# Kernel tuning notes

Hardware: AMD Instinct MI355X
Metric: run time of the kernel (lower is better)

The kernel has to match this reference:

```python
import jax, jax.numpy as jnp
import numpy as np

B, N, DIM = 64, 197, 768
NUM_HEAD, HEAD_DIM = 12, 64
SCALE = HEAD_DIM ** -0.5
WS = (14, 14)
NUM_REL = (2 * WS[0] - 1) * (2 * WS[1] - 1) + 3  # 732


def _relative_position_index():
    coords = np.stack(np.meshgrid(np.arange(WS[0]), np.arange(WS[1]), indexing='ij'))  # (2, Wh, Ww)
    cf = coords.reshape(2, -1)                              # (2, Wh*Ww)
    rel = (cf[:, :, None] - cf[:, None, :]).transpose(1, 2, 0).astype(np.int64)
    rel[:, :, 0] += WS[0] - 1
    rel[:, :, 1] += WS[1] - 1
    rel[:, :, 0] *= 2 * WS[1] - 1
    idx = np.zeros((WS[0] * WS[1] + 1,) * 2, dtype=np.int32)
    idx[1:, 1:] = rel.sum(-1)
    idx[0, :] = NUM_REL - 3
    idx[:, 0] = NUM_REL - 2
    idx[0, 0] = NUM_REL - 1
    return idx


def setup_inputs() -> dict:
    key = jax.random.key(0)
    k1, k2, k3, k4 = jax.random.split(key, 4)
    x = jax.random.normal(k1, (B, N, DIM), dtype=jnp.float32)
    qkv_w = jax.random.normal(k2, (3 * DIM, DIM), dtype=jnp.float32) * (DIM ** -0.5)
    q_bias = jnp.zeros((DIM,), dtype=jnp.float32)
    v_bias = jnp.zeros((DIM,), dtype=jnp.float32)
    rpb_table = jax.random.normal(k3, (NUM_REL, NUM_HEAD), dtype=jnp.float32) * 0.02
    proj_w = jax.random.normal(k4, (DIM, DIM), dtype=jnp.float32) * (DIM ** -0.5)
    proj_b = jnp.zeros((DIM,), dtype=jnp.float32)
    rel_index = jnp.asarray(_relative_position_index())
    return {"x": x, "qkv_w": qkv_w, "q_bias": q_bias, "v_bias": v_bias,
            "rpb_table": rpb_table, "proj_w": proj_w, "proj_b": proj_b,
            "rel_index": rel_index}


def reference(x, qkv_w, q_bias, v_bias, rpb_table, proj_w, proj_b, rel_index):
    b, n, c = x.shape
    # qkv projection with [q_bias, 0, v_bias] bias layout
    qkv_bias = jnp.concatenate([q_bias, jnp.zeros_like(v_bias), v_bias])
    qkv = x @ qkv_w.T + qkv_bias                               # (B, N, 3*C)
    qkv = qkv.reshape(b, n, 3, NUM_HEAD, HEAD_DIM).transpose(2, 0, 3, 1, 4)
    q, k, v = qkv[0] * SCALE, qkv[1], qkv[2]                   # (B, H, N, hd)
    attn = jnp.einsum('bhqd,bhkd->bhqk', q, k)                 # (B, H, N, N)
    # relative position bias gather: table[(N,N)] -> (N, N, H) -> (H, N, N)
    bias = rpb_table[rel_index].transpose(2, 0, 1)
    attn = jax.nn.softmax(attn + bias[None], axis=-1)
    out = jnp.einsum('bhqk,bhkd->bhqd', attn, v)               # (B, H, N, hd)
    out = out.transpose(0, 2, 1, 3).reshape(b, n, -1)
    return out @ proj_w.T + proj_b
```

## Files before the change

kernel.cpp:

```cpp
#include <hip/hip_runtime.h>


#define B_    64
#define N_    197
#define DIM_  768
#define H_    12
#define HD_   64
#define M_TOT (B_ * N_)

#define ST_A0   0
#define ST_A1   13312
#define ST_A2   26624
#define ST_B0   39936
#define ST_B1   52224
#define ST_B2   64512
#define OFF_Q   0
#define OFF_K   13312
#define OFF_VT  26624
#define LDS_TOT 76800

typedef __attribute__((ext_vector_type(8))) short bf8;
typedef __attribute__((ext_vector_type(4))) float f4;
typedef __attribute__((ext_vector_type(4))) unsigned short us4;

__device__ __forceinline__ unsigned short f2bf(float f) {
    unsigned u = __float_as_uint(f);
    u = (u + 0x7fffu + ((u >> 16) & 1u)) >> 16;
    return (unsigned short)u;
}

__device__ __forceinline__ void gl2lds16(const unsigned short* g, unsigned short* l) {
    __builtin_amdgcn_global_load_lds(
        (const __attribute__((address_space(1))) void*)g,
        (__attribute__((address_space(3))) void*)l, 16, 0, 0);
}

__device__ __forceinline__ int qkaddr(int row, int col) {
    return row * 64 + ((((col >> 3) ^ row) & 7) << 3) + (col & 7);
}
__device__ __forceinline__ int vtaddr(int d, int k) {
    int s = k >> 3;
    int s2 = (s < 24) ? ((s & 24) | ((s ^ d) & 7)) : (24 + ((s ^ d) & 3));
    return d * 224 + (s2 << 3) + (k & 7);
}

__global__ void k_prep(const float* __restrict__ x, const float* __restrict__ qkvw,
                       const float* __restrict__ projw, const float* __restrict__ rpb,
                       const int* __restrict__ relidx,
                       unsigned short* __restrict__ x_bf, unsigned short* __restrict__ qkvw_bf,
                       unsigned short* __restrict__ projw_bf, float* __restrict__ bias_hqk) {
    const int T = gridDim.x * blockDim.x;
    const int tid = blockIdx.x * blockDim.x + threadIdx.x;
    for (int i = tid; i < M_TOT * DIM_ / 4; i += T) {
        float4 v = ((const float4*)x)[i];
        us4 o = {f2bf(v.x), f2bf(v.y), f2bf(v.z), f2bf(v.w)};
        ((us4*)x_bf)[i] = o;
    }
    for (int i = tid; i < 3 * DIM_ * DIM_ / 4; i += T) {
        float4 v = ((const float4*)qkvw)[i];
        us4 o = {f2bf(v.x), f2bf(v.y), f2bf(v.z), f2bf(v.w)};
        ((us4*)qkvw_bf)[i] = o;
    }
    for (int i = tid; i < DIM_ * DIM_ / 4; i += T) {
        float4 v = ((const float4*)projw)[i];
        us4 o = {f2bf(v.x), f2bf(v.y), f2bf(v.z), f2bf(v.w)};
        ((us4*)projw_bf)[i] = o;
    }
    for (int i = tid; i < H_ * N_ * N_; i += T) {
        int h = i / (N_ * N_), qk = i - h * (N_ * N_);
        bias_hqk[i] = rpb[relidx[qk] * H_ + h];
    }
}

__global__ __launch_bounds__(1024) void k_fused(const unsigned short* __restrict__ X,
                                                const unsigned short* __restrict__ Wqkv,
                                                const float* __restrict__ qb,
                                                const float* __restrict__ vbias,
                                                const float* __restrict__ bias_hqk,
                                                unsigned short* __restrict__ att_ws) {
    __shared__ unsigned short lds[LDS_TOT];

    const int t = threadIdx.x;
    const int w = t >> 6, lane = t & 63, ln = lane & 15, quad = lane >> 4;
    const int wm = w >> 2, wn = w & 3;
    const int srl = lane >> 3;
    const int src8 = (lane & 7) ^ srl;

    const int gid = blockIdx.x;
    const int local = gid >> 3;
    const int b = (gid & 7) * 8 + (local & 7);
    const int h = local >> 3;

    const unsigned short* xb = X + (size_t)b * 197 * 768;

    auto stage = [&](int kt, int aOfs, int bOfs) {
#pragma unroll
        for (int i = 0; i < 4; ++i) {
            int idx = (15 - w) + 16 * i;
            if (idx >= 50) break;
            if (idx < 26) {
                int tok = 8 * idx + srl;
                if (tok > 196) tok = 196;
                gl2lds16(xb + (size_t)tok * 768 + kt * 64 + src8 * 8,
                         &lds[aOfs + idx * 512]);
            } else {
                int bb = idx - 26;
                int rr = 8 * bb + srl;
                gl2lds16(Wqkv + (size_t)((rr >> 6) * 768 + h * 64 + (rr & 63)) * 768
                              + kt * 64 + src8 * 8,
                         &lds[bOfs + bb * 512]);
            }
        }
    };

    f4 acc[4][3] = {};

    auto compute = [&](int aOfs, int bOfs) {
#pragma unroll
        for (int ks = 0; ks < 2; ++ks) {
            bf8 bfr[3];
#pragma unroll
            for (int tl = 0; tl < 3; ++tl) {
                int rr = (wn * 3 + tl) * 16 + ln;
                int slot = (ks * 4 + quad) ^ (rr & 7);
                bfr[tl] = *(const bf8*)&lds[bOfs + rr * 64 + slot * 8];
            }
            __builtin_amdgcn_s_setprio(1);
#pragma unroll
            for (int mi = 0; mi < 4; ++mi) {
                int mt = wm + 4 * mi;
                if (mt >= 13) continue;
                int row = mt * 16 + ln;
                int slot = (ks * 4 + quad) ^ (row & 7);
                bf8 af = *(const bf8*)&lds[aOfs + row * 64 + slot * 8];
#pragma unroll
                for (int tl = 0; tl < 3; ++tl)
                    acc[mi][tl] = __builtin_amdgcn_mfma_f32_16x16x32_bf16(
                        af, bfr[tl], acc[mi][tl], 0, 0, 0);
            }
            __builtin_amdgcn_s_setprio(0);
        }
    };

    const int stA[3] = {ST_A0, ST_A1, ST_A2};
    const int stB[3] = {ST_B0, ST_B1, ST_B2};
    stage(0, ST_A0, ST_B0);
    stage(1, ST_A1, ST_B1);
#pragma unroll
    for (int kt = 0; kt < 12; ++kt) {
        if (kt < 11) { __asm__ __volatile__("s_waitcnt vmcnt(3)" ::: "memory"); }
        else         { __asm__ __volatile__("s_waitcnt vmcnt(0)" ::: "memory"); }
        __builtin_amdgcn_sched_barrier(0);
        __builtin_amdgcn_s_barrier();
        __builtin_amdgcn_sched_barrier(0);
        if (kt + 2 < 12) stage(kt + 2, stA[(kt + 2) % 3], stB[(kt + 2) % 3]);
        compute(stA[kt % 3], stB[kt % 3]);
    }
    __syncthreads();

#pragma unroll
    for (int tl = 0; tl < 3; ++tl) {
        int tn = wn * 3 + tl;
        int p = tn >> 2;
        int col = (tn & 3) * 16 + ln;
        int d = h * 64 + col;
        float bj = (p == 0) ? qb[d] : (p == 2) ? vbias[d] : 0.0f;
#pragma unroll
        for (int mi = 0; mi < 4; ++mi) {
            int mt = wm + 4 * mi;
            if (mt >= 13) continue;
#pragma unroll
            for (int r = 0; r < 4; ++r) {
                int row = mt * 16 + quad * 4 + r;
                float v = acc[mi][tl][r];
                if (p == 0)      lds[OFF_Q + qkaddr(row, col)] = f2bf((v + bj) * 0.125f);
                else if (p == 1) lds[OFF_K + qkaddr(row, col)] = f2bf(v);
                else             lds[OFF_VT + vtaddr(col, row)] = f2bf(v + bj);
            }
        }
    }
    for (int idx = t; idx < 64 * 16; idx += 1024) {
        int d = idx >> 4, k = 208 + (idx & 15);
        lds[OFF_VT + vtaddr(d, k)] = 0;
    }
    __syncthreads();

    const float* bp = bias_hqk + (size_t)h * 197 * 197;

    for (int mt = w; mt < 13; mt += 16) {
        bf8 qa[2];
#pragma unroll
        for (int ks = 0; ks < 2; ++ks)
            qa[ks] = *(const bf8*)&lds[OFF_Q + qkaddr(mt * 16 + ln, ks * 32 + quad * 8)];

        f4 sacc[13];
#pragma unroll
        for (int nt = 0; nt < 13; ++nt) sacc[nt] = (f4){0.f, 0.f, 0.f, 0.f};
        __builtin_amdgcn_s_setprio(1);
#pragma unroll
        for (int nt = 0; nt < 13; ++nt) {
#pragma unroll
            for (int ks = 0; ks < 2; ++ks) {
                bf8 ka = *(const bf8*)&lds[OFF_K + qkaddr(nt * 16 + ln, ks * 32 + quad * 8)];
                sacc[nt] = __builtin_amdgcn_mfma_f32_16x16x32_bf16(ka, qa[ks], sacc[nt], 0, 0, 0);
            }
        }
        __builtin_amdgcn_s_setprio(0);

        int qg = mt * 16 + ln;
        const float* brow = bp + (size_t)(qg < 197 ? qg : 196) * 197;
        float mx = -3.0e38f;
#pragma unroll
        for (int nt = 0; nt < 13; ++nt)
#pragma unroll
            for (int r = 0; r < 4; ++r) {
                int kg = nt * 16 + quad * 4 + r;
                float s = (kg < 197) ? (sacc[nt][r] + brow[kg]) : -3.0e38f;
                sacc[nt][r] = s;
                mx = fmaxf(mx, s);
            }
        mx = fmaxf(mx, __shfl_xor(mx, 16, 64));
        mx = fmaxf(mx, __shfl_xor(mx, 32, 64));
        float sum = 0.f;
#pragma unroll
        for (int nt = 0; nt < 13; ++nt)
#pragma unroll
            for (int r = 0; r < 4; ++r) {
                float pv = __expf(sacc[nt][r] - mx);
                sacc[nt][r] = pv;
                sum += pv;
            }
        sum += __shfl_xor(sum, 16, 64);
        sum += __shfl_xor(sum, 32, 64);
        float inv = 1.0f / sum;

        unsigned pk[14][2];
#pragma unroll
        for (int nt = 0; nt < 13; ++nt) {
            pk[nt][0] = (unsigned)f2bf(sacc[nt][0] * inv) |
                        ((unsigned)f2bf(sacc[nt][1] * inv) << 16);
            pk[nt][1] = (unsigned)f2bf(sacc[nt][2] * inv) |
                        ((unsigned)f2bf(sacc[nt][3] * inv) << 16);
        }
        pk[13][0] = 0; pk[13][1] = 0;

        const int sA = (((lane & 15) | ((lane & 16) << 1)) << 2);
        const int sB = sA + 64;
        const bool hi = (lane & 32) != 0;
        f4 o[4];
#pragma unroll
        for (int j = 0; j < 4; ++j) o[j] = (f4){0.f, 0.f, 0.f, 0.f};
#pragma unroll
        for (int ks = 0; ks < 7; ++ks) {
            int b0 = __builtin_amdgcn_ds_bpermute(sA, (int)pk[2 * ks][0]);
            int b1 = __builtin_amdgcn_ds_bpermute(sA, (int)pk[2 * ks][1]);
            int b2 = __builtin_amdgcn_ds_bpermute(sB, (int)pk[2 * ks][0]);
            int b3 = __builtin_amdgcn_ds_bpermute(sB, (int)pk[2 * ks][1]);
            int c0 = __builtin_amdgcn_ds_bpermute(sA, (int)pk[2 * ks + 1][0]);
            int c1 = __builtin_amdgcn_ds_bpermute(sA, (int)pk[2 * ks + 1][1]);
            int c2 = __builtin_amdgcn_ds_bpermute(sB, (int)pk[2 * ks + 1][0]);
            int c3 = __builtin_amdgcn_ds_bpermute(sB, (int)pk[2 * ks + 1][1]);
            union { int u[4]; bf8 v; } uu;
            uu.u[0] = hi ? c0 : b0;
            uu.u[1] = hi ? c1 : b1;
            uu.u[2] = hi ? c2 : b2;
            uu.u[3] = hi ? c3 : b3;
            __builtin_amdgcn_s_setprio(1);
#pragma unroll
            for (int j = 0; j < 4; ++j) {
                bf8 vf = *(const bf8*)&lds[OFF_VT + vtaddr(j * 16 + ln, ks * 32 + quad * 8)];
                o[j] = __builtin_amdgcn_mfma_f32_16x16x32_bf16(uu.v, vf, o[j], 0, 0, 0);
            }
            __builtin_amdgcn_s_setprio(0);
        }
#pragma unroll
        for (int j = 0; j < 4; ++j)
#pragma unroll
            for (int r = 0; r < 4; ++r) {
                int tok = mt * 16 + quad * 4 + r;
                if (tok < 197)
                    att_ws[((size_t)b * 197 + tok) * 768 + h * 64 + j * 16 + ln] = f2bf(o[j][r]);
            }
    }
}

#define PJ_BUF 8192

__device__ __forceinline__ void pj_stage(const unsigned short* __restrict__ A,
                                         const unsigned short* __restrict__ Bm,
                                         int bm, int bn, int kt, int w, int srl, int src8,
                                         unsigned short* buf) {
#pragma unroll
    for (int i = 0; i < 2; ++i) {
        int idx = w * 2 + i;
        int gr = bm * 128 + 2 * (idx * 8 + srl) + (src8 >> 2);
        if (gr > M_TOT - 1) gr = M_TOT - 1;
        gl2lds16(A + (size_t)gr * 768 + kt * 32 + (src8 & 3) * 8,
                 &buf[idx * 512]);
        int gc = bn * 128 + 2 * (idx * 8 + srl) + (src8 >> 2);
        gl2lds16(Bm + (size_t)gc * 768 + kt * 32 + (src8 & 3) * 8,
                 &buf[4096 + idx * 512]);
    }
}

__device__ __forceinline__ void pj_compute(const unsigned short* buf,
                                           int wm, int wn, int ln, int quad, f4 (*acc)[4]) {
    bf8 af[4], bfr[4];
#pragma unroll
    for (int i = 0; i < 4; ++i) {
        int row = wm * 64 + i * 16 + ln;
        int sr = row >> 1;
        int slot = (((row & 1) << 2) | quad) ^ (sr & 7);
        af[i] = *(const bf8*)&buf[sr * 64 + slot * 8];
    }
#pragma unroll
    for (int j = 0; j < 4; ++j) {
        int row = wn * 64 + j * 16 + ln;
        int sr = row >> 1;
        int slot = (((row & 1) << 2) | quad) ^ (sr & 7);
        bfr[j] = *(const bf8*)&buf[4096 + sr * 64 + slot * 8];
    }
    __builtin_amdgcn_s_setprio(1);
#pragma unroll
    for (int i = 0; i < 4; ++i)
#pragma unroll
        for (int j = 0; j < 4; ++j)
            acc[i][j] = __builtin_amdgcn_mfma_f32_16x16x32_bf16(af[i], bfr[j], acc[i][j], 0, 0, 0);
    __builtin_amdgcn_s_setprio(0);
}

__global__ __launch_bounds__(256, 3) void k_proj(const unsigned short* __restrict__ A,
                                                 const unsigned short* __restrict__ Bm,
                                                 const float* __restrict__ pb,
                                                 float* __restrict__ out) {
    __shared__ unsigned short plds[3 * PJ_BUF];
    const int t = threadIdx.x;
    const int w = t >> 6, lane = t & 63, ln = lane & 15, quad = lane >> 4;
    const int wm = w & 1, wn = w >> 1;

    const int gid = blockIdx.x;
    const int panel = gid / 48, rem = gid - panel * 48;
    const int pm0 = panel * 8;
    const int psz = (99 - pm0 < 8) ? (99 - pm0) : 8;
    const int bm = pm0 + rem % psz;
    const int bn = rem / psz;

    const int srl = lane >> 3;
    const int src8 = (lane & 7) ^ srl;

    f4 acc[4][4] = {};

    pj_stage(A, Bm, bm, bn, 0, w, srl, src8, &plds[0]);
    pj_stage(A, Bm, bm, bn, 1, w, srl, src8, &plds[PJ_BUF]);
#pragma unroll
    for (int kt = 0; kt < 24; ++kt) {
        if (kt < 23) { __asm__ __volatile__("s_waitcnt vmcnt(4)" ::: "memory"); }
        else         { __asm__ __volatile__("s_waitcnt vmcnt(0)" ::: "memory"); }
        __builtin_amdgcn_sched_barrier(0);
        __builtin_amdgcn_s_barrier();
        __builtin_amdgcn_sched_barrier(0);
        if (kt + 2 < 24) pj_stage(A, Bm, bm, bn, kt + 2, w, srl, src8,
                                  &plds[((kt + 2) % 3) * PJ_BUF]);
        pj_compute(&plds[(kt % 3) * PJ_BUF], wm, wn, ln, quad, acc);
    }

#pragma unroll
    for (int i = 0; i < 4; ++i) {
#pragma unroll
        for (int r = 0; r < 4; ++r) {
            int row_g = bm * 128 + wm * 64 + i * 16 + quad * 4 + r;
            if (row_g >= M_TOT) continue;
#pragma unroll
            for (int j = 0; j < 4; ++j) {
                int col_g = bn * 128 + wn * 64 + j * 16 + ln;
                out[(size_t)row_g * 768 + col_g] = acc[i][j][r] + pb[col_g];
            }
        }
    }
}

extern "C" void kernel_launch(void* const* d_in, const int* in_sizes, int n_in,
                              void* d_out, int out_size, void* d_ws, size_t ws_size,
                              hipStream_t stream) {
    const float* x     = (const float*)d_in[0];
    const float* qkvw  = (const float*)d_in[1];
    const float* qb    = (const float*)d_in[2];
    const float* vb    = (const float*)d_in[3];
    const float* rpb   = (const float*)d_in[4];
    const float* projw = (const float*)d_in[5];
    const float* pb    = (const float*)d_in[6];
    const int*   ridx  = (const int*)d_in[7];
    float* out = (float*)d_out;

    char* ws = (char*)d_ws;
    size_t off = 0;
    auto alloc = [&](size_t bytes) -> void* {
        void* p = ws + off;
        off = (off + bytes + 255) & ~(size_t)255;
        return p;
    };
    unsigned short* x_bf     = (unsigned short*)alloc((size_t)M_TOT * DIM_ * 2);
    unsigned short* qkvw_bf  = (unsigned short*)alloc((size_t)3 * DIM_ * DIM_ * 2);
    unsigned short* projw_bf = (unsigned short*)alloc((size_t)DIM_ * DIM_ * 2);
    float*          bias_h   = (float*)alloc((size_t)H_ * N_ * N_ * 4);
    unsigned short* att_ws   = (unsigned short*)alloc((size_t)(M_TOT + 64) * DIM_ * 2);
    (void)ws_size; (void)in_sizes; (void)n_in; (void)out_size;

    k_prep<<<1200, 256, 0, stream>>>(x, qkvw, projw, rpb, ridx,
                                     x_bf, qkvw_bf, projw_bf, bias_h);
    k_fused<<<768, 1024, 0, stream>>>(x_bf, qkvw_bf, qb, vb, bias_h, att_ws);
    k_proj<<<594, 256, 0, stream>>>(att_ws, projw_bf, pb, out);
}
```

Before: 207.9 us.

## Fuse fp32-to-bf16 conversion and bias gather into GEMM kernels, drop prep kernel

Removes the separate prep kernel that converted x and the weights to bf16 and materialised the per-head relative-position bias. The fused and projection kernels now load fp32 directly into registers, convert to bf16 and write into LDS, using a two-buffer register-staged pipeline instead of a three-stage direct global-to-LDS load. The softmax gathers the bias through rel_index and the table inline. This saves a kernel launch and the round trip of the bf16 copies, but each of the 12 heads rereads fp32 x, which doubles load bytes, and it loses the async LDS-load overlap.

```diff
diff --git a/kernel.cpp b/kernel.cpp
--- a/kernel.cpp
+++ b/kernel.cpp
@@ -9,15 +9,13 @@
 #define M_TOT (B_ * N_)
 
 #define ST_A0   0
-#define ST_A1   13312
-#define ST_A2   26624
-#define ST_B0   39936
-#define ST_B1   52224
-#define ST_B2   64512
+#define ST_B0   13312
+#define ST_A1   25600
+#define ST_B1   38912
 #define OFF_Q   0
 #define OFF_K   13312
 #define OFF_VT  26624
-#define LDS_TOT 76800
+#define LDS_TOT 51200
 
 typedef __attribute__((ext_vector_type(8))) short bf8;
 typedef __attribute__((ext_vector_type(4))) float f4;
@@ -29,12 +27,6 @@
     return (unsigned short)u;
 }
 
-__device__ __forceinline__ void gl2lds16(const unsigned short* g, unsigned short* l) {
-    __builtin_amdgcn_global_load_lds(
-        (const __attribute__((address_space(1))) void*)g,
-        (__attribute__((address_space(3))) void*)l, 16, 0, 0);
-}
-
 __device__ __forceinline__ int qkaddr(int row, int col) {
     return row * 64 + ((((col >> 3) ^ row) & 7) << 3) + (col & 7);
 }
@@ -44,39 +36,20 @@
     return d * 224 + (s2 << 3) + (k & 7);
 }
 
-__global__ void k_prep(const float* __restrict__ x, const float* __restrict__ qkvw,
-                       const float* __restrict__ projw, const float* __restrict__ rpb,
-                       const int* __restrict__ relidx,
-                       unsigned short* __restrict__ x_bf, unsigned short* __restrict__ qkvw_bf,
-                       unsigned short* __restrict__ projw_bf, float* __restrict__ bias_hqk) {
-    const int T = gridDim.x * blockDim.x;
-    const int tid = blockIdx.x * blockDim.x + threadIdx.x;
-    for (int i = tid; i < M_TOT * DIM_ / 4; i += T) {
-        float4 v = ((const float4*)x)[i];
-        us4 o = {f2bf(v.x), f2bf(v.y), f2bf(v.z), f2bf(v.w)};
-        ((us4*)x_bf)[i] = o;
-    }
-    for (int i = tid; i < 3 * DIM_ * DIM_ / 4; i += T) {
-        float4 v = ((const float4*)qkvw)[i];
-        us4 o = {f2bf(v.x), f2bf(v.y), f2bf(v.z), f2bf(v.w)};
-        ((us4*)qkvw_bf)[i] = o;
-    }
-    for (int i = tid; i < DIM_ * DIM_ / 4; i += T) {
-        float4 v = ((const float4*)projw)[i];
-        us4 o = {f2bf(v.x), f2bf(v.y), f2bf(v.z), f2bf(v.w)};
-        ((us4*)projw_bf)[i] = o;
-    }
-    for (int i = tid; i < H_ * N_ * N_; i += T) {
-        int h = i / (N_ * N_), qk = i - h * (N_ * N_);
-        bias_hqk[i] = rpb[relidx[qk] * H_ + h];
-    }
-}
-
-__global__ __launch_bounds__(1024) void k_fused(const unsigned short* __restrict__ X,
-                                                const unsigned short* __restrict__ Wqkv,
+union pk16 { us4 u[2]; uint4 q; };
+__device__ __forceinline__ uint4 cvt8(const float4& lo, const float4& hi) {
+    pk16 p;
+    p.u[0] = (us4){f2bf(lo.x), f2bf(lo.y), f2bf(lo.z), f2bf(lo.w)};
+    p.u[1] = (us4){f2bf(hi.x), f2bf(hi.y), f2bf(hi.z), f2bf(hi.w)};
+    return p.q;
+}
+
+__global__ __launch_bounds__(1024) void k_fused(const float* __restrict__ X32,
+                                                const float* __restrict__ W32,
                                                 const float* __restrict__ qb,
                                                 const float* __restrict__ vbias,
-                                                const float* __restrict__ bias_hqk,
+                                                const float* __restrict__ rpb,
+                                                const int* __restrict__ relidx,
                                                 unsigned short* __restrict__ att_ws) {
     __shared__ unsigned short lds[LDS_TOT];
 
@@ -91,25 +64,40 @@
     const int b = (gid & 7) * 8 + (local & 7);
     const int h = local >> 3;
 
-    const unsigned short* xb = X + (size_t)b * 197 * 768;
-
-    auto stage = [&](int kt, int aOfs, int bOfs) {
+    const float* xb = X32 + (size_t)b * 197 * 768;
+
+    float4 rg[8];
+
+    auto ldreg = [&](int kt) {
 #pragma unroll
         for (int i = 0; i < 4; ++i) {
             int idx = (15 - w) + 16 * i;
             if (idx >= 50) break;
+            const float* src;
             if (idx < 26) {
                 int tok = 8 * idx + srl;
                 if (tok > 196) tok = 196;
-                gl2lds16(xb + (size_t)tok * 768 + kt * 64 + src8 * 8,
-                         &lds[aOfs + idx * 512]);
+                src = xb + (size_t)tok * 768 + kt * 64 + src8 * 8;
             } else {
                 int bb = idx - 26;
                 int rr = 8 * bb + srl;
-                gl2lds16(Wqkv + (size_t)((rr >> 6) * 768 + h * 64 + (rr & 63)) * 768
-                              + kt * 64 + src8 * 8,
-                         &lds[bOfs + bb * 512]);
-            }
+                src = W32 + (size_t)((rr >> 6) * 768 + h * 64 + (rr & 63)) * 768
+                          + kt * 64 + src8 * 8;
+            }
+            rg[2 * i]     = *(const float4*)(src);
+            rg[2 * i + 1] = *(const float4*)(src + 4);
+        }
+    };
+    auto wrreg = [&](int aOfs, int bOfs) {
+#pragma unroll
+        for (int i = 0; i < 4; ++i) {
+            int idx = (15 - w) + 16 * i;
+            if (idx >= 50) break;
+            uint4 v = cvt8(rg[2 * i], rg[2 * i + 1]);
+            unsigned short* dst = (idx < 26)
+                ? &lds[aOfs + idx * 512 + lane * 8]
+                : &lds[bOfs + (idx - 26) * 512 + lane * 8];
+            *(uint4*)dst = v;
         }
     };
 
@@ -142,19 +130,22 @@
         }
     };
 
-    const int stA[3] = {ST_A0, ST_A1, ST_A2};
-    const int stB[3] = {ST_B0, ST_B1, ST_B2};
-    stage(0, ST_A0, ST_B0);
-    stage(1, ST_A1, ST_B1);
+    ldreg(0);
+    __asm__ __volatile__("s_waitcnt vmcnt(0)" ::: "memory");
+    wrreg(ST_A0, ST_B0);
+    __syncthreads();
 #pragma unroll
     for (int kt = 0; kt < 12; ++kt) {
-        if (kt < 11) { __asm__ __volatile__("s_waitcnt vmcnt(3)" ::: "memory"); }
-        else         { __asm__ __volatile__("s_waitcnt vmcnt(0)" ::: "memory"); }
+        if (kt + 1 < 12) ldreg(kt + 1);
+        compute((kt & 1) ? ST_A1 : ST_A0, (kt & 1) ? ST_B1 : ST_B0);
+        if (kt + 1 < 12) {
+            __asm__ __volatile__("s_waitcnt vmcnt(0)" ::: "memory");
+            wrreg((kt & 1) ? ST_A0 : ST_A1, (kt & 1) ? ST_B0 : ST_B1);
+        }
+        __builtin_amdgcn_sched_barrier(0);
+        __asm__ __volatile__("s_waitcnt lgkmcnt(0)" ::: "memory");
         __builtin_amdgcn_sched_barrier(0);
         __builtin_amdgcn_s_barrier();
-        __builtin_amdgcn_sched_barrier(0);
-        if (kt + 2 < 12) stage(kt + 2, stA[(kt + 2) % 3], stB[(kt + 2) % 3]);
-        compute(stA[kt % 3], stB[kt % 3]);
     }
     __syncthreads();
 
@@ -185,8 +176,6 @@
     }
     __syncthreads();
 
-    const float* bp = bias_hqk + (size_t)h * 197 * 197;
-
     for (int mt = w; mt < 13; mt += 16) {
         bf8 qa[2];
 #pragma unroll
@@ -208,14 +197,15 @@
         __builtin_amdgcn_s_setprio(0);
 
         int qg = mt * 16 + ln;
-        const float* brow = bp + (size_t)(qg < 197 ? qg : 196) * 197;
+        const int* relrow = relidx + (size_t)(qg < 197 ? qg : 196) * 197;
         float mx = -3.0e38f;
 #pragma unroll
         for (int nt = 0; nt < 13; ++nt)
 #pragma unroll
             for (int r = 0; r < 4; ++r) {
                 int kg = nt * 16 + quad * 4 + r;
-                float s = (kg < 197) ? (sacc[nt][r] + brow[kg]) : -3.0e38f;
+                float s = (kg < 197) ? (sacc[nt][r] + rpb[relrow[kg] * H_ + h])
+                                     : -3.0e38f;
                 sacc[nt][r] = s;
                 mx = fmaxf(mx, s);
             }
@@ -286,54 +276,11 @@
 
 #define PJ_BUF 8192
 
-__device__ __forceinline__ void pj_stage(const unsigned short* __restrict__ A,
-                                         const unsigned short* __restrict__ Bm,
-                                         int bm, int bn, int kt, int w, int srl, int src8,
-                                         unsigned short* buf) {
-#pragma unroll
-    for (int i = 0; i < 2; ++i) {
-        int idx = w * 2 + i;
-        int gr = bm * 128 + 2 * (idx * 8 + srl) + (src8 >> 2);
-        if (gr > M_TOT - 1) gr = M_TOT - 1;
-        gl2lds16(A + (size_t)gr * 768 + kt * 32 + (src8 & 3) * 8,
-                 &buf[idx * 512]);
-        int gc = bn * 128 + 2 * (idx * 8 + srl) + (src8 >> 2);
-        gl2lds16(Bm + (size_t)gc * 768 + kt * 32 + (src8 & 3) * 8,
-                 &buf[4096 + idx * 512]);
-    }
-}
-
-__device__ __forceinline__ void pj_compute(const unsigned short* buf,
-                                           int wm, int wn, int ln, int quad, f4 (*acc)[4]) {
-    bf8 af[4], bfr[4];
-#pragma unroll
-    for (int i = 0; i < 4; ++i) {
-        int row = wm * 64 + i * 16 + ln;
-        int sr = row >> 1;
-        int slot = (((row & 1) << 2) | quad) ^ (sr & 7);
-        af[i] = *(const bf8*)&buf[sr * 64 + slot * 8];
-    }
-#pragma unroll
-    for (int j = 0; j < 4; ++j) {
-        int row = wn * 64 + j * 16 + ln;
-        int sr = row >> 1;
-        int slot = (((row & 1) << 2) | quad) ^ (sr & 7);
-        bfr[j] = *(const bf8*)&buf[4096 + sr * 64 + slot * 8];
-    }
-    __builtin_amdgcn_s_setprio(1);
-#pragma unroll
-    for (int i = 0; i < 4; ++i)
-#pragma unroll
-        for (int j = 0; j < 4; ++j)
-            acc[i][j] = __builtin_amdgcn_mfma_f32_16x16x32_bf16(af[i], bfr[j], acc[i][j], 0, 0, 0);
-    __builtin_amdgcn_s_setprio(0);
-}
-
 __global__ __launch_bounds__(256, 3) void k_proj(const unsigned short* __restrict__ A,
-                                                 const unsigned short* __restrict__ Bm,
+                                                 const float* __restrict__ Bw32,
                                                  const float* __restrict__ pb,
                                                  float* __restrict__ out) {
-    __shared__ unsigned short plds[3 * PJ_BUF];
+    __shared__ unsigned short plds[2 * PJ_BUF];
     const int t = threadIdx.x;
     const int w = t >> 6, lane = t & 63, ln = lane & 15, quad = lane >> 4;
     const int wm = w & 1, wn = w >> 1;
@@ -348,20 +295,73 @@
     const int srl = lane >> 3;
     const int src8 = (lane & 7) ^ srl;
 
+    uint4  ra[2];
+    float4 rb[4];
+
+    auto pld = [&](int kt) {
+#pragma unroll
+        for (int i = 0; i < 2; ++i) {
+            int idx = w * 2 + i;
+            int gr = bm * 128 + 2 * (idx * 8 + srl) + (src8 >> 2);
+            if (gr > M_TOT - 1) gr = M_TOT - 1;
+            ra[i] = *(const uint4*)(A + (size_t)gr * 768 + kt * 32 + (src8 & 3) * 8);
+            int gc = bn * 128 + 2 * (idx * 8 + srl) + (src8 >> 2);
+            const float* s = Bw32 + (size_t)gc * 768 + kt * 32 + (src8 & 3) * 8;
+            rb[2 * i]     = *(const float4*)(s);
+            rb[2 * i + 1] = *(const float4*)(s + 4);
+        }
+    };
+    auto pwr = [&](unsigned short* buf) {
+#pragma unroll
+        for (int i = 0; i < 2; ++i) {
+            int idx = w * 2 + i;
+            *(uint4*)&buf[idx * 512 + lane * 8] = ra[i];
+            *(uint4*)&buf[4096 + idx * 512 + lane * 8] = cvt8(rb[2 * i], rb[2 * i + 1]);
+        }
+    };
+    auto pcomp = [&](const unsigned short* buf, f4 (*acc)[4]) {
+        bf8 af[4], bfr[4];
+#pragma unroll
+        for (int i = 0; i < 4; ++i) {
+            int row = wm * 64 + i * 16 + ln;
+            int sr = row >> 1;
+            int slot = (((row & 1) << 2) | quad) ^ (sr & 7);
+            af[i] = *(const bf8*)&buf[sr * 64 + slot * 8];
+        }
+#pragma unroll
+        for (int j = 0; j < 4; ++j) {
+            int row = wn * 64 + j * 16 + ln;
+            int sr = row >> 1;
+            int slot = (((row & 1) << 2) | quad) ^ (sr & 7);
+            bfr[j] = *(const bf8*)&buf[4096 + sr * 64 + slot * 8];
+        }
+        __builtin_amdgcn_s_setprio(1);
+#pragma unroll
+        for (int i = 0; i < 4; ++i)
+#pragma unroll
+            for (int j = 0; j < 4; ++j)
+                acc[i][j] = __builtin_amdgcn_mfma_f32_16x16x32_bf16(af[i], bfr[j], acc[i][j], 0, 0, 0);
+        __builtin_amdgcn_s_setprio(0);
+    };
+
     f4 acc[4][4] = {};
 
-    pj_stage(A, Bm, bm, bn, 0, w, srl, src8, &plds[0]);
-    pj_stage(A, Bm, bm, bn, 1, w, srl, src8, &plds[PJ_BUF]);
+    pld(0);
+    __asm__ __volatile__("s_waitcnt vmcnt(0)" ::: "memory");
+    pwr(&plds[0]);
+    __syncthreads();
 #pragma unroll
     for (int kt = 0; kt < 24; ++kt) {
-        if (kt < 23) { __asm__ __volatile__("s_waitcnt vmcnt(4)" ::: "memory"); }
-        else         { __asm__ __volatile__("s_waitcnt vmcnt(0)" ::: "memory"); }
+        if (kt + 1 < 24) pld(kt + 1);
+        pcomp(&plds[(kt & 1) * PJ_BUF], acc);
+        if (kt + 1 < 24) {
+            __asm__ __volatile__("s_waitcnt vmcnt(0)" ::: "memory");
+            pwr(&plds[((kt + 1) & 1) * PJ_BUF]);
+        }
+        __builtin_amdgcn_sched_barrier(0);
+        __asm__ __volatile__("s_waitcnt lgkmcnt(0)" ::: "memory");
         __builtin_amdgcn_sched_barrier(0);
         __builtin_amdgcn_s_barrier();
-        __builtin_amdgcn_sched_barrier(0);
-        if (kt + 2 < 24) pj_stage(A, Bm, bm, bn, kt + 2, w, srl, src8,
-                                  &plds[((kt + 2) % 3) * PJ_BUF]);
-        pj_compute(&plds[(kt % 3) * PJ_BUF], wm, wn, ln, quad, acc);
     }
 
 #pragma unroll
@@ -399,15 +399,9 @@
         off = (off + bytes + 255) & ~(size_t)255;
         return p;
     };
-    unsigned short* x_bf     = (unsigned short*)alloc((size_t)M_TOT * DIM_ * 2);
-    unsigned short* qkvw_bf  = (unsigned short*)alloc((size_t)3 * DIM_ * DIM_ * 2);
-    unsigned short* projw_bf = (unsigned short*)alloc((size_t)DIM_ * DIM_ * 2);
-    float*          bias_h   = (float*)alloc((size_t)H_ * N_ * N_ * 4);
-    unsigned short* att_ws   = (unsigned short*)alloc((size_t)(M_TOT + 64) * DIM_ * 2);
+    unsigned short* att_ws = (unsigned short*)alloc((size_t)(M_TOT + 64) * DIM_ * 2);
     (void)ws_size; (void)in_sizes; (void)n_in; (void)out_size;
 
-    k_prep<<<1200, 256, 0, stream>>>(x, qkvw, projw, rpb, ridx,
-                                     x_bf, qkvw_bf, projw_bf, bias_h);
-    k_fused<<<768, 1024, 0, stream>>>(x_bf, qkvw_bf, qb, vb, bias_h, att_ws);
-    k_proj<<<594, 256, 0, stream>>>(att_ws, projw_bf, pb, out);
-}
+    k_fused<<<768, 1024, 0, stream>>>(x, qkvw, qb, vb, rpb, ridx, att_ws);
+    k_proj<<<594, 256, 0, stream>>>(att_ws, projw, pb, out);
+}
```

After: 299.8 us. 44.2% more time.
